# Kernel tuning notes

Hardware: AMD Instinct MI355X
Metric: run time of the kernel (lower is better)

Reference implementation:

```python
import jax, jax.numpy as jnp
import numpy as np

B, S, D = 16, 2048, 128


def setup_inputs() -> dict:
    k = jax.random.key(0)
    k1, k2, k3, k4 = jax.random.split(k, 4)
    query = jax.random.normal(k1, (B, S, D), dtype=jnp.float32)
    key = jax.random.normal(k2, (B, S, D), dtype=jnp.float32)
    value = jax.random.normal(k3, (B, S, D), dtype=jnp.float32)
    # per-query tensor-valued inverse scale; shift away from zero for stable division
    inv_scale_factor = jax.random.uniform(k4, (B, S, 1), dtype=jnp.float32) + 0.5
    dropout_p = jnp.float32(0.1)
    return {"query": query, "key": key, "value": value,
            "inv_scale_factor": inv_scale_factor, "dropout_p": dropout_p}


def reference(query, key, value, inv_scale_factor, dropout_p):
    # QK^T: [B, Sq, Sk]
    qk = jnp.einsum('bqd,bkd->bqk', query, key)
    # tensor-valued scale divide (broadcast [B, Sq, 1] over keys)
    scaled_qk = qk / inv_scale_factor
    softmax_qk = jax.nn.softmax(scaled_qk, axis=-1)
    # dropout with a fixed RNG key (deterministic reference)
    keep_prob = 1.0 - dropout_p
    mask = jax.random.bernoulli(jax.random.key(42), keep_prob, softmax_qk.shape)
    dropout_qk = jnp.where(mask, softmax_qk / keep_prob, jnp.float32(0.0))
    # AV: [B, Sq, Dv]
    return jnp.einsum('bqk,bkv->bqv', dropout_qk, value)
```

## Files before the change

### kernel.cpp

```cpp
#include <hip/hip_runtime.h>
#include <hip/hip_bf16.h>
#include <stdint.h>


#define B_ 16
#define S_ 2048
#define D_ 128
#define TQ 64
#define TK 64
#define KSTR 136
#define VSTR 72
#define PSTR 72

typedef float f32x4 __attribute__((ext_vector_type(4)));
typedef short b16x8 __attribute__((ext_vector_type(8)));

union U4B8 { uint32_t u[4]; b16x8 v; };
union F32R { float4 q[8]; float f[32]; };
union F16R { float4 q[4]; float f[16]; };

__device__ __forceinline__ uint32_t pk_bf16(float a, float b) {
  union { __hip_bfloat162 h; uint32_t u; } c;
  c.h = __float22bfloat162_rn(make_float2(a, b));
  return c.u;
}

#define DPP_ROR(x, ctrl) \
  __int_as_float(__builtin_amdgcn_update_dpp(0, __float_as_int(x), (ctrl), 0xf, 0xf, true))
__device__ __forceinline__ float row16_max(float x) {
  x = fmaxf(x, DPP_ROR(x, 0x128));
  x = fmaxf(x, DPP_ROR(x, 0x124));
  x = fmaxf(x, DPP_ROR(x, 0x122));
  x = fmaxf(x, DPP_ROR(x, 0x121));
  return x;
}
__device__ __forceinline__ float row16_sum(float x) {
  x += DPP_ROR(x, 0x128);
  x += DPP_ROR(x, 0x124);
  x += DPP_ROR(x, 0x122);
  x += DPP_ROR(x, 0x121);
  return x;
}

__device__ __forceinline__ uint2 threefry2x32_0_42(uint32_t x0, uint32_t x1) {
  const uint32_t k0 = 0u, k1 = 42u;
  const uint32_t k2 = 0x1BD11BDAu ^ k0 ^ k1;
  x0 += k0; x1 += k1;
#define TFR(r) { x0 += x1; x1 = __builtin_rotateleft32(x1, r); x1 ^= x0; }
  TFR(13) TFR(15) TFR(26) TFR(6)
  x0 += k1; x1 += k2 + 1u;
  TFR(17) TFR(29) TFR(16) TFR(24)
  x0 += k2; x1 += k0 + 2u;
  TFR(13) TFR(15) TFR(26) TFR(6)
  x0 += k0; x1 += k1 + 3u;
  TFR(17) TFR(29) TFR(16) TFR(24)
  x0 += k1; x1 += k2 + 4u;
  TFR(13) TFR(15) TFR(26) TFR(6)
  x0 += k2; x1 += k0 + 5u;
#undef TFR
  return make_uint2(x0, x1);
}

__device__ __forceinline__ uint32_t jax_bits(uint32_t j) {
  const uint2 tf = threefry2x32_0_42(0u, j);
  return tf.x ^ tf.y;
}

__global__ __launch_bounds__(256, 2)
void attn_mfma_kernel(const float* __restrict__ Q, const float* __restrict__ K,
                      const float* __restrict__ V, const float* __restrict__ ISF,
                      const float* __restrict__ DP, float* __restrict__ OUT) {
  __shared__ __align__(16) short sKhi[TK * KSTR];
  __shared__ __align__(16) short sKlo[TK * KSTR];
  __shared__ __align__(16) short sVT[D_ * VSTR];
  __shared__ __align__(16) short sP[4 * 16 * PSTR];

  const int t    = threadIdx.x;
  const int w    = t >> 6;
  const int lane = t & 63;
  const int l15  = lane & 15;
  const int quad = lane >> 4;
  const int b    = blockIdx.y;
  const int qw   = blockIdx.x * TQ + w * 16;

  const float kp = 1.0f - DP[0];
  const uint32_t TH9 = (__float_as_uint(1.0f + kp) & 0x7FFFFFu) << 9;

  float m_[4], l_[4];
  uint32_t jq[4];
  #pragma unroll
  for (int r = 0; r < 4; ++r) {
    m_[r] = -INFINITY;
    l_[r] = 0.0f;
    jq[r] = ((uint32_t)b << 22) + (uint32_t)(qw + quad * 4 + r) * (uint32_t)S_;
  }

  b16x8 qhi[4], qlo[4];
  {
    const float qs = 1.4426950408889634f / ISF[b * S_ + qw + l15];
    const float* qp = Q + ((size_t)(b * S_ + qw + l15)) * D_;
    #pragma unroll
    for (int c = 0; c < 4; ++c) {
      const float4 a = *(const float4*)(qp + c * 32 + quad * 8);
      const float4 d = *(const float4*)(qp + c * 32 + quad * 8 + 4);
      float xs[8] = {a.x, a.y, a.z, a.w, d.x, d.y, d.z, d.w};
      U4B8 hi, lo;
      #pragma unroll
      for (int p = 0; p < 4; ++p) {
        const float x0 = xs[2 * p] * qs, x1 = xs[2 * p + 1] * qs;
        const uint32_t h = pk_bf16(x0, x1);
        const float r0 = x0 - __uint_as_float(h << 16);
        const float r1 = x1 - __uint_as_float(h & 0xFFFF0000u);
        hi.u[p] = h;
        lo.u[p] = pk_bf16(r0, r1);
      }
      qhi[c] = hi.v;
      qlo[c] = lo.v;
    }
  }

  f32x4 accO[8];
  #pragma unroll
  for (int i = 0; i < 8; ++i) accO[i] = (f32x4){0.f, 0.f, 0.f, 0.f};

  short* const pwv = &sP[w * 16 * PSTR];

  const int krow = t >> 2, kcol = (t & 3) * 32;
  const int vkey = 2 * (t & 31), vseg = (t >> 5) * 16;

  F32R kreg;
  F16R vreg0, vreg1;

#define ISSUE_LOADS(KT)                                                        \
  {                                                                            \
    const float4* gk4 = (const float4*)(K +                                    \
        ((size_t)(b * S_ + (KT) * TK + krow)) * D_ + kcol);                    \
    _Pragma("unroll") for (int i = 0; i < 8; ++i) kreg.q[i] = gk4[i];          \
    const float4* gv4 = (const float4*)(V +                                    \
        ((size_t)(b * S_ + (KT) * TK + vkey)) * D_ + vseg);                    \
    _Pragma("unroll") for (int i = 0; i < 4; ++i) {                            \
      vreg0.q[i] = gv4[i];                                                     \
      vreg1.q[i] = gv4[i + 32];                \
    }                                                                          \
  }

  ISSUE_LOADS(0)

  for (int kt = 0; kt < S_ / TK; ++kt) {
    __syncthreads();

    {
      short* kh = &sKhi[krow * KSTR + kcol];
      short* kl = &sKlo[krow * KSTR + kcol];
      #pragma unroll
      for (int g = 0; g < 4; ++g) {
        U4B8 hi, lo;
        #pragma unroll
        for (int p = 0; p < 4; ++p) {
          const float x0 = kreg.f[g * 8 + 2 * p], x1 = kreg.f[g * 8 + 2 * p + 1];
          const uint32_t h = pk_bf16(x0, x1);
          const float r0 = x0 - __uint_as_float(h << 16);
          const float r1 = x1 - __uint_as_float(h & 0xFFFF0000u);
          hi.u[p] = h;
          lo.u[p] = pk_bf16(r0, r1);
        }
        *(b16x8*)&kh[g * 8] = hi.v;
        *(b16x8*)&kl[g * 8] = lo.v;
      }
    }
    {
      #pragma unroll
      for (int d = 0; d < 16; ++d)
        *(uint32_t*)&sVT[(vseg + d) * VSTR + vkey] = pk_bf16(vreg0.f[d], vreg1.f[d]);
    }
    __syncthreads();

    if (kt + 1 < S_ / TK) ISSUE_LOADS(kt + 1)

    f32x4 s[4];
    #pragma unroll
    for (int n = 0; n < 4; ++n) {
      f32x4 acc = (f32x4){0.f, 0.f, 0.f, 0.f};
      #pragma unroll
      for (int c = 0; c < 4; ++c) {
        const b16x8 bh = *(const b16x8*)&sKhi[(n * 16 + l15) * KSTR + c * 32 + quad * 8];
        const b16x8 bl = *(const b16x8*)&sKlo[(n * 16 + l15) * KSTR + c * 32 + quad * 8];
        acc = __builtin_amdgcn_mfma_f32_16x16x32_bf16(qhi[c], bh, acc, 0, 0, 0);
        acc = __builtin_amdgcn_mfma_f32_16x16x32_bf16(qhi[c], bl, acc, 0, 0, 0);
        acc = __builtin_amdgcn_mfma_f32_16x16x32_bf16(qlo[c], bh, acc, 0, 0, 0);
      }
      s[n] = acc;
    }

    float mx[4];
    #pragma unroll
    for (int r = 0; r < 4; ++r) {
      mx[r] = row16_max(fmaxf(fmaxf(s[0][r], s[1][r]), fmaxf(s[2][r], s[3][r])));
    }
    int changed = 0;
    #pragma unroll
    for (int r = 0; r < 4; ++r) changed |= (mx[r] > m_[r]);
    if (__ballot(changed) != 0ull) {
      #pragma unroll
      for (int r = 0; r < 4; ++r) {
        const float mnew = fmaxf(m_[r], mx[r]);
        const float alpha = __builtin_amdgcn_exp2f(m_[r] - mnew);
        m_[r] = mnew;
        l_[r] *= alpha;
        #pragma unroll
        for (int i = 0; i < 8; ++i) accO[i][r] *= alpha;
      }
    }
    float rs[4];
    #pragma unroll
    for (int r = 0; r < 4; ++r) {
      float lr = 0.f;
      #pragma unroll
      for (int n = 0; n < 4; ++n) {
        const float p = __builtin_amdgcn_exp2f(s[n][r] - m_[r]);
        s[n][r] = p;
        lr += p;
      }
      rs[r] = lr;
    }
    #pragma unroll
    for (int r = 0; r < 4; ++r) l_[r] += row16_sum(rs[r]);

    #pragma unroll
    for (int n = 0; n < 4; ++n) {
      const int col = n * 16 + l15;
      const uint32_t jcol = (uint32_t)(kt * TK + col);
      float pf[4];
      #pragma unroll
      for (int r = 0; r < 4; ++r) {
        const uint32_t bits = jax_bits(jq[r] + jcol);
        pf[r] = (bits < TH9) ? s[n][r] : 0.0f;
      }
      const uint32_t pk01 = pk_bf16(pf[0], pf[1]);
      const uint32_t pk23 = pk_bf16(pf[2], pf[3]);
      pwv[(quad * 4 + 0) * PSTR + col] = (short)(uint16_t)pk01;
      pwv[(quad * 4 + 1) * PSTR + col] = (short)(uint16_t)(pk01 >> 16);
      pwv[(quad * 4 + 2) * PSTR + col] = (short)(uint16_t)pk23;
      pwv[(quad * 4 + 3) * PSTR + col] = (short)(uint16_t)(pk23 >> 16);
    }
    __threadfence_block();

    #pragma unroll
    for (int ks = 0; ks < 2; ++ks) {
      const b16x8 ap = *(const b16x8*)&pwv[l15 * PSTR + ks * 32 + quad * 8];
      #pragma unroll
      for (int d8 = 0; d8 < 8; ++d8) {
        const b16x8 bv = *(const b16x8*)&sVT[(d8 * 16 + l15) * VSTR + ks * 32 + quad * 8];
        accO[d8] = __builtin_amdgcn_mfma_f32_16x16x32_bf16(ap, bv, accO[d8], 0, 0, 0);
      }
    }
  }
#undef ISSUE_LOADS

  float inv[4];
  #pragma unroll
  for (int r = 0; r < 4; ++r) inv[r] = 1.0f / (l_[r] * kp);
  float* op = OUT + ((size_t)(b * S_ + qw)) * D_;
  #pragma unroll
  for (int d8 = 0; d8 < 8; ++d8) {
    #pragma unroll
    for (int r = 0; r < 4; ++r)
      op[(quad * 4 + r) * D_ + d8 * 16 + l15] = accO[d8][r] * inv[r];
  }
}

extern "C" void kernel_launch(void* const* d_in, const int* in_sizes, int n_in,
                              void* d_out, int out_size, void* d_ws, size_t ws_size,
                              hipStream_t stream) {
  const float* q   = (const float*)d_in[0];
  const float* k   = (const float*)d_in[1];
  const float* v   = (const float*)d_in[2];
  const float* isf = (const float*)d_in[3];
  const float* dp  = (const float*)d_in[4];
  float* out = (float*)d_out;

  dim3 grid(S_ / TQ, B_);
  attn_mfma_kernel<<<grid, dim3(256), 0, stream>>>(q, k, v, isf, dp, out);
}
```

Baseline: 330.7 us.

## Switch QK to single fp16 MFMA, split key tile across two wave groups

```diff
diff --git a/kernel.cpp b/kernel.cpp
--- a/kernel.cpp
+++ b/kernel.cpp
@@ -1,5 +1,4 @@
 #include <hip/hip_runtime.h>
-#include <hip/hip_bf16.h>
 #include <stdint.h>
 
 
@@ -10,20 +9,11 @@
 #define TK 64
 #define KSTR 136
 #define VSTR 72
-#define PSTR 72
+#define PSTR 40
 
 typedef float f32x4 __attribute__((ext_vector_type(4)));
-typedef short b16x8 __attribute__((ext_vector_type(8)));
-
-union U4B8 { uint32_t u[4]; b16x8 v; };
-union F32R { float4 q[8]; float f[32]; };
-union F16R { float4 q[4]; float f[16]; };
-
-__device__ __forceinline__ uint32_t pk_bf16(float a, float b) {
-  union { __hip_bfloat162 h; uint32_t u; } c;
-  c.h = __float22bfloat162_rn(make_float2(a, b));
-  return c.u;
-}
+typedef _Float16 f16x8 __attribute__((ext_vector_type(8)));
+typedef _Float16 f16x2 __attribute__((ext_vector_type(2)));
 
 #define DPP_ROR(x, ctrl) \
   __int_as_float(__builtin_amdgcn_update_dpp(0, __float_as_int(x), (ctrl), 0xf, 0xf, true))
@@ -66,22 +56,27 @@
   return tf.x ^ tf.y;
 }
 
-__global__ __launch_bounds__(256, 2)
+__global__ __launch_bounds__(512, 4)
 void attn_mfma_kernel(const float* __restrict__ Q, const float* __restrict__ K,
                       const float* __restrict__ V, const float* __restrict__ ISF,
                       const float* __restrict__ DP, float* __restrict__ OUT) {
-  __shared__ __align__(16) short sKhi[TK * KSTR];
-  __shared__ __align__(16) short sKlo[TK * KSTR];
-  __shared__ __align__(16) short sVT[D_ * VSTR];
-  __shared__ __align__(16) short sP[4 * 16 * PSTR];
+  __shared__ __align__(16) char smem[46080];
+  _Float16* const sK  = (_Float16*)smem;
+  _Float16* const sVT = (_Float16*)(smem + 17408);
+  _Float16* const sP  = (_Float16*)(smem + 35840);
+  float* const sO1 = (float*)smem;
+  float* const sM1 = (float*)(smem + 32768);
+  float* const sL1 = (float*)(smem + 33024);
 
   const int t    = threadIdx.x;
-  const int w    = t >> 6;
   const int lane = t & 63;
   const int l15  = lane & 15;
   const int quad = lane >> 4;
+  const int w    = t >> 6;
+  const int qg   = w & 3;
+  const int kph  = w >> 2;
   const int b    = blockIdx.y;
-  const int qw   = blockIdx.x * TQ + w * 16;
+  const int qw   = blockIdx.x * TQ + qg * 16;
 
   const float kp = 1.0f - DP[0];
   const uint32_t TH9 = (__float_as_uint(1.0f + kp) & 0x7FFFFFu) << 9;
@@ -95,27 +90,19 @@
     jq[r] = ((uint32_t)b << 22) + (uint32_t)(qw + quad * 4 + r) * (uint32_t)S_;
   }
 
-  b16x8 qhi[4], qlo[4];
+  f16x8 qf[4];
   {
     const float qs = 1.4426950408889634f / ISF[b * S_ + qw + l15];
     const float* qp = Q + ((size_t)(b * S_ + qw + l15)) * D_;
     #pragma unroll
     for (int c = 0; c < 4; ++c) {
       const float4 a = *(const float4*)(qp + c * 32 + quad * 8);
-      const float4 d = *(const float4*)(qp + c * 32 + quad * 8 + 4);
-      float xs[8] = {a.x, a.y, a.z, a.w, d.x, d.y, d.z, d.w};
-      U4B8 hi, lo;
-      #pragma unroll
-      for (int p = 0; p < 4; ++p) {
-        const float x0 = xs[2 * p] * qs, x1 = xs[2 * p + 1] * qs;
-        const uint32_t h = pk_bf16(x0, x1);
-        const float r0 = x0 - __uint_as_float(h << 16);
-        const float r1 = x1 - __uint_as_float(h & 0xFFFF0000u);
-        hi.u[p] = h;
-        lo.u[p] = pk_bf16(r0, r1);
-      }
-      qhi[c] = hi.v;
-      qlo[c] = lo.v;
+      const float4 d2 = *(const float4*)(qp + c * 32 + quad * 8 + 4);
+      const float xs[8] = {a.x, a.y, a.z, a.w, d2.x, d2.y, d2.z, d2.w};
+      f16x8 h;
+      #pragma unroll
+      for (int j = 0; j < 8; ++j) h[j] = (_Float16)(xs[j] * qs);
+      qf[c] = h;
     }
   }
 
@@ -123,80 +110,58 @@
   #pragma unroll
   for (int i = 0; i < 8; ++i) accO[i] = (f32x4){0.f, 0.f, 0.f, 0.f};
 
-  short* const pwv = &sP[w * 16 * PSTR];
-
-  const int krow = t >> 2, kcol = (t & 3) * 32;
-  const int vkey = 2 * (t & 31), vseg = (t >> 5) * 16;
-
-  F32R kreg;
-  F16R vreg0, vreg1;
-
-#define ISSUE_LOADS(KT)                                                        \
-  {                                                                            \
-    const float4* gk4 = (const float4*)(K +                                    \
-        ((size_t)(b * S_ + (KT) * TK + krow)) * D_ + kcol);                    \
-    _Pragma("unroll") for (int i = 0; i < 8; ++i) kreg.q[i] = gk4[i];          \
-    const float4* gv4 = (const float4*)(V +                                    \
-        ((size_t)(b * S_ + (KT) * TK + vkey)) * D_ + vseg);                    \
-    _Pragma("unroll") for (int i = 0; i < 4; ++i) {                            \
-      vreg0.q[i] = gv4[i];                                                     \
-      vreg1.q[i] = gv4[i + 32];                \
-    }                                                                          \
-  }
-
-  ISSUE_LOADS(0)
+  _Float16* const pwv = &sP[w * 16 * PSTR];
+
+  const int krow = t >> 3, kcol = (t & 7) * 16;
+  const int vp = t & 31, dseg = (t >> 5) * 8;
 
   for (int kt = 0; kt < S_ / TK; ++kt) {
     __syncthreads();
 
     {
-      short* kh = &sKhi[krow * KSTR + kcol];
-      short* kl = &sKlo[krow * KSTR + kcol];
-      #pragma unroll
-      for (int g = 0; g < 4; ++g) {
-        U4B8 hi, lo;
+      const float* gk = K + ((size_t)(b * S_ + kt * TK + krow)) * D_ + kcol;
+      float kf[16];
+      #pragma unroll
+      for (int i = 0; i < 4; ++i) *(float4*)&kf[i * 4] = *(const float4*)(gk + i * 4);
+      #pragma unroll
+      for (int g = 0; g < 2; ++g) {
+        f16x8 h;
         #pragma unroll
-        for (int p = 0; p < 4; ++p) {
-          const float x0 = kreg.f[g * 8 + 2 * p], x1 = kreg.f[g * 8 + 2 * p + 1];
-          const uint32_t h = pk_bf16(x0, x1);
-          const float r0 = x0 - __uint_as_float(h << 16);
-          const float r1 = x1 - __uint_as_float(h & 0xFFFF0000u);
-          hi.u[p] = h;
-          lo.u[p] = pk_bf16(r0, r1);
-        }
-        *(b16x8*)&kh[g * 8] = hi.v;
-        *(b16x8*)&kl[g * 8] = lo.v;
+        for (int j = 0; j < 8; ++j) h[j] = (_Float16)kf[g * 8 + j];
+        *(f16x8*)&sK[krow * KSTR + kcol + g * 8] = h;
       }
     }
     {
-      #pragma unroll
-      for (int d = 0; d < 16; ++d)
-        *(uint32_t*)&sVT[(vseg + d) * VSTR + vkey] = pk_bf16(vreg0.f[d], vreg1.f[d]);
+      const float* gv = V + ((size_t)(b * S_ + kt * TK + 2 * vp)) * D_ + dseg;
+      float v0[8], v1[8];
+      #pragma unroll
+      for (int i = 0; i < 2; ++i) {
+        *(float4*)&v0[i * 4] = *(const float4*)(gv + i * 4);
+        *(float4*)&v1[i * 4] = *(const float4*)(gv + D_ + i * 4);
+      }
+      #pragma unroll
+      for (int d = 0; d < 8; ++d) {
+        f16x2 h = {(_Float16)v0[d], (_Float16)v1[d]};
+        *(f16x2*)&sVT[(dseg + d) * VSTR + 2 * vp] = h;
+      }
     }
     __syncthreads();
 
-    if (kt + 1 < S_ / TK) ISSUE_LOADS(kt + 1)
-
-    f32x4 s[4];
-    #pragma unroll
-    for (int n = 0; n < 4; ++n) {
+    f32x4 s[2];
+    #pragma unroll
+    for (int n = 0; n < 2; ++n) {
       f32x4 acc = (f32x4){0.f, 0.f, 0.f, 0.f};
       #pragma unroll
       for (int c = 0; c < 4; ++c) {
-        const b16x8 bh = *(const b16x8*)&sKhi[(n * 16 + l15) * KSTR + c * 32 + quad * 8];
-        const b16x8 bl = *(const b16x8*)&sKlo[(n * 16 + l15) * KSTR + c * 32 + quad * 8];
-        acc = __builtin_amdgcn_mfma_f32_16x16x32_bf16(qhi[c], bh, acc, 0, 0, 0);
-        acc = __builtin_amdgcn_mfma_f32_16x16x32_bf16(qhi[c], bl, acc, 0, 0, 0);
-        acc = __builtin_amdgcn_mfma_f32_16x16x32_bf16(qlo[c], bh, acc, 0, 0, 0);
+        const f16x8 bh = *(const f16x8*)&sK[(kph * 32 + n * 16 + l15) * KSTR + c * 32 + quad * 8];
+        acc = __builtin_amdgcn_mfma_f32_16x16x32_f16(qf[c], bh, acc, 0, 0, 0);
       }
       s[n] = acc;
     }
 
     float mx[4];
     #pragma unroll
-    for (int r = 0; r < 4; ++r) {
-      mx[r] = row16_max(fmaxf(fmaxf(s[0][r], s[1][r]), fmaxf(s[2][r], s[3][r])));
-    }
+    for (int r = 0; r < 4; ++r) mx[r] = row16_max(fmaxf(s[0][r], s[1][r]));
     int changed = 0;
     #pragma unroll
     for (int r = 0; r < 4; ++r) changed |= (mx[r] > m_[r]);
@@ -211,61 +176,76 @@
         for (int i = 0; i < 8; ++i) accO[i][r] *= alpha;
       }
     }
-    float rs[4];
     #pragma unroll
     for (int r = 0; r < 4; ++r) {
-      float lr = 0.f;
-      #pragma unroll
-      for (int n = 0; n < 4; ++n) {
-        const float p = __builtin_amdgcn_exp2f(s[n][r] - m_[r]);
-        s[n][r] = p;
-        lr += p;
-      }
-      rs[r] = lr;
-    }
-    #pragma unroll
-    for (int r = 0; r < 4; ++r) l_[r] += row16_sum(rs[r]);
-
-    #pragma unroll
-    for (int n = 0; n < 4; ++n) {
+      const float p0 = __builtin_amdgcn_exp2f(s[0][r] - m_[r]);
+      const float p1 = __builtin_amdgcn_exp2f(s[1][r] - m_[r]);
+      s[0][r] = p0; s[1][r] = p1;
+      l_[r] += row16_sum(p0 + p1);
+    }
+
+    #pragma unroll
+    for (int n = 0; n < 2; ++n) {
       const int col = n * 16 + l15;
-      const uint32_t jcol = (uint32_t)(kt * TK + col);
-      float pf[4];
+      const uint32_t jcol = (uint32_t)(kt * TK + kph * 32 + col);
       #pragma unroll
       for (int r = 0; r < 4; ++r) {
         const uint32_t bits = jax_bits(jq[r] + jcol);
-        pf[r] = (bits < TH9) ? s[n][r] : 0.0f;
-      }
-      const uint32_t pk01 = pk_bf16(pf[0], pf[1]);
-      const uint32_t pk23 = pk_bf16(pf[2], pf[3]);
-      pwv[(quad * 4 + 0) * PSTR + col] = (short)(uint16_t)pk01;
-      pwv[(quad * 4 + 1) * PSTR + col] = (short)(uint16_t)(pk01 >> 16);
-      pwv[(quad * 4 + 2) * PSTR + col] = (short)(uint16_t)pk23;
-      pwv[(quad * 4 + 3) * PSTR + col] = (short)(uint16_t)(pk23 >> 16);
+        const float pf = (bits < TH9) ? s[n][r] : 0.0f;
+        pwv[(quad * 4 + r) * PSTR + col] = (_Float16)pf;
+      }
     }
     __threadfence_block();
 
-    #pragma unroll
-    for (int ks = 0; ks < 2; ++ks) {
-      const b16x8 ap = *(const b16x8*)&pwv[l15 * PSTR + ks * 32 + quad * 8];
+    {
+      const f16x8 ap = *(const f16x8*)&pwv[l15 * PSTR + quad * 8];
       #pragma unroll
       for (int d8 = 0; d8 < 8; ++d8) {
-        const b16x8 bv = *(const b16x8*)&sVT[(d8 * 16 + l15) * VSTR + ks * 32 + quad * 8];
-        accO[d8] = __builtin_amdgcn_mfma_f32_16x16x32_bf16(ap, bv, accO[d8], 0, 0, 0);
-      }
-    }
-  }
-#undef ISSUE_LOADS
-
-  float inv[4];
-  #pragma unroll
-  for (int r = 0; r < 4; ++r) inv[r] = 1.0f / (l_[r] * kp);
-  float* op = OUT + ((size_t)(b * S_ + qw)) * D_;
-  #pragma unroll
-  for (int d8 = 0; d8 < 8; ++d8) {
-    #pragma unroll
-    for (int r = 0; r < 4; ++r)
-      op[(quad * 4 + r) * D_ + d8 * 16 + l15] = accO[d8][r] * inv[r];
+        const f16x8 bv = *(const f16x8*)&sVT[(d8 * 16 + l15) * VSTR + kph * 32 + quad * 8];
+        accO[d8] = __builtin_amdgcn_mfma_f32_16x16x32_f16(ap, bv, accO[d8], 0, 0, 0);
+      }
+    }
+  }
+
+  __syncthreads();
+  if (kph == 1) {
+    if (l15 == 0) {
+      #pragma unroll
+      for (int r = 0; r < 4; ++r) {
+        sM1[qg * 16 + quad * 4 + r] = m_[r];
+        sL1[qg * 16 + quad * 4 + r] = l_[r];
+      }
+    }
+    #pragma unroll
+    for (int d8 = 0; d8 < 8; ++d8) {
+      #pragma unroll
+      for (int r = 0; r < 4; ++r)
+        sO1[qg * 2048 + (quad * 4 + r) * D_ + d8 * 16 + l15] = accO[d8][r];
+    }
+  }
+  __syncthreads();
+  if (kph == 0) {
+    float a0s[4], a1s[4];
+    #pragma unroll
+    for (int r = 0; r < 4; ++r) {
+      const float m1  = sM1[qg * 16 + quad * 4 + r];
+      const float l1v = sL1[qg * 16 + quad * 4 + r];
+      const float mf = fmaxf(m_[r], m1);
+      const float a0 = __builtin_amdgcn_exp2f(m_[r] - mf);
+      const float a1 = __builtin_amdgcn_exp2f(m1 - mf);
+      const float inv = 1.0f / ((a0 * l_[r] + a1 * l1v) * kp);
+      a0s[r] = a0 * inv;
+      a1s[r] = a1 * inv;
+    }
+    float* op = OUT + ((size_t)(b * S_ + qw)) * D_;
+    #pragma unroll
+    for (int d8 = 0; d8 < 8; ++d8) {
+      #pragma unroll
+      for (int r = 0; r < 4; ++r) {
+        const float o1 = sO1[qg * 2048 + (quad * 4 + r) * D_ + d8 * 16 + l15];
+        op[(quad * 4 + r) * D_ + d8 * 16 + l15] = accO[d8][r] * a0s[r] + o1 * a1s[r];
+      }
+    }
   }
 }
 
@@ -280,5 +260,5 @@
   float* out = (float*)d_out;
 
   dim3 grid(S_ / TQ, B_);
-  attn_mfma_kernel<<<grid, dim3(256), 0, stream>>>(q, k, v, isf, dp, out);
-}
+  attn_mfma_kernel<<<grid, dim3(512), 0, stream>>>(q, k, v, isf, dp, out);
+}
```

Result: slower. 338.1 us (+2.2%).
